# Kernel tuning notes

Hardware: AMD Instinct MI355X
Metric: run time of the kernel (lower is better)

Reference implementation:

```python
import jax, jax.numpy as jnp
import numpy as np

N = 50000      # nodes
E = 400000     # edges (avg degree 8)
N_IN = 256     # n_in_chan
N_HID = 256    # n_hid_chan


def gcn_conv(x, src, dst, W, b, n):
    """PyG GCNConv: D^{-1/2}(A+I)D^{-1/2} X W^T + b (add_self_loops=True, unit weights)."""
    h = x @ W.T                                           # [n, out]
    # degree over A + I: each node has a self loop (the initial ones) plus in-edges
    deg = jnp.ones((n,), h.dtype).at[dst].add(1.0)        # [n]
    dinv = jax.lax.rsqrt(deg)                             # deg >= 1 always
    norm = dinv[src] * dinv[dst]                          # [E]
    agg = jnp.zeros_like(h).at[dst].add(h[src] * norm[:, None])
    agg = agg + h * (dinv * dinv)[:, None]                # self-loop term, norm = dinv_i^2
    return agg + b


def setup_inputs() -> dict:
    key = jax.random.key(0)
    k1, k2, k3, k4 = jax.random.split(key, 4)
    x = jax.random.normal(k1, (N, N_IN + N_HID), dtype=jnp.float32)
    edge_index = jax.random.randint(k2, (2, E), 0, N, dtype=jnp.int64)
    s1 = 1.0 / np.sqrt(N_IN + N_HID)
    s2 = 1.0 / np.sqrt(N_HID)
    W1 = jax.random.normal(k3, (N_HID, N_IN + N_HID), dtype=jnp.float32) * s1
    W2 = jax.random.normal(k4, (N_HID, N_HID), dtype=jnp.float32) * s2
    b1 = jnp.zeros((N_HID,), jnp.float32)
    b2 = jnp.zeros((N_HID,), jnp.float32)
    return {"x": x, "edge_index": edge_index, "W1": W1, "b1": b1, "W2": W2, "b2": b2}


def reference(x, edge_index, W1, b1, W2, b2):
    src, dst = edge_index[0], edge_index[1]
    h = jax.nn.relu(gcn_conv(x, src, dst, W1, b1, N))
    return gcn_conv(h, src, dst, W2, b2, N)
```

## Files before the change

kernel.cpp:

```cpp
#include <hip/hip_runtime.h>
#include <hip/hip_bf16.h>

#define NN 50000
#define CH 256
#define SLOTS 96
#define G1K 512
#define G2K 256

typedef unsigned short u16;
typedef unsigned int   u32;

using short8 = __attribute__((ext_vector_type(8))) short;
using u16x8  = __attribute__((ext_vector_type(8))) unsigned short;
using f32x4  = __attribute__((ext_vector_type(4))) float;

static __device__ __forceinline__ float4 ld4(const float* p){ return *(const float4*)p; }

static __device__ __forceinline__ u16 f2b(float f){
  u32 u = __float_as_uint(f);
  u = (u + 0x7fffu + ((u >> 16) & 1u)) >> 16;
  return (u16)u;
}
static __device__ __forceinline__ float b2f(u16 b){
  return __uint_as_float(((u32)b) << 16);
}
static __device__ __forceinline__ int pkbf(float lo, float hi){
  __hip_bfloat162 h = __float22bfloat162_rn(make_float2(lo, hi));
  int r; __builtin_memcpy(&r, &h, 4); return r;
}

static __device__ __forceinline__ void gload_lds16(const u16* g, u16* l){
  __builtin_amdgcn_global_load_lds((const __attribute__((address_space(1))) void*)g,
                                   (__attribute__((address_space(3))) void*)l, 16, 0, 0);
}

#define WBAR(vm) do{ \
    asm volatile("s_waitcnt vmcnt(" #vm ") lgkmcnt(0)" ::: "memory"); \
    __builtin_amdgcn_s_barrier(); \
  }while(0)


__global__ void ell_build_kernel(const int* __restrict__ src, const int* __restrict__ dst,
                                 int* __restrict__ deg, int* __restrict__ ell, int E,
                                 const float* __restrict__ W1, u16* __restrict__ W1bf, int w1n4,
                                 const float* __restrict__ W2, u16* __restrict__ W2bf, int w2n4){
  int T = gridDim.x * 256;
  int g = blockIdx.x*256 + threadIdx.x;
  if (g < E){
    int d = dst[g];
    int pos = atomicAdd(&deg[d], 1);
    if (pos < SLOTS) ell[(size_t)d*SLOTS + pos] = src[g];
  }
  for (int i = g; i < w1n4; i += T){
    float4 v = ld4(W1 + (size_t)i*4);
    ushort4 o; o.x=f2b(v.x); o.y=f2b(v.y); o.z=f2b(v.z); o.w=f2b(v.w);
    *(ushort4*)(W1bf + (size_t)i*4) = o;
  }
  for (int i = g; i < w2n4; i += T){
    float4 v = ld4(W2 + (size_t)i*4);
    ushort4 o; o.x=f2b(v.x); o.y=f2b(v.y); o.z=f2b(v.z); o.w=f2b(v.w);
    *(ushort4*)(W2bf + (size_t)i*4) = o;
  }
}


#define G1_GLB(kt, bb) do{ \
    gload_lds16(gb0 + (kt)*32, &Bs[bb][wave*512]); \
    gload_lds16(gb1 + (kt)*32, &Bs[bb][2048 + wave*512]); \
  }while(0)

#define G1_LA(S, k0) do{ \
    A##S##a = ld4(ga0 + (k0)); A##S##b = ld4(ga0 + (k0) + 4); \
    A##S##c = ld4(ga1 + (k0)); A##S##d = ld4(ga1 + (k0) + 4); \
  }while(0)

#define G1_SA(S) do{ \
    int4 _w0 = { pkbf(A##S##a.x,A##S##a.y), pkbf(A##S##a.z,A##S##a.w), \
                 pkbf(A##S##b.x,A##S##b.y), pkbf(A##S##b.z,A##S##b.w) }; \
    int4 _w1 = { pkbf(A##S##c.x,A##S##c.y), pkbf(A##S##c.z,A##S##c.w), \
                 pkbf(A##S##d.x,A##S##d.y), pkbf(A##S##d.z,A##S##d.w) }; \
    *(int4*)&As[S][aoff0] = _w0; \
    *(int4*)&As[S][aoff1] = _w1; \
  }while(0)

#define G1_COMP(ra, rb) do{ \
    short8 af[4], bq[4]; \
    _Pragma("unroll") \
    for (int i=0;i<4;i++) af[i] = *(const short8*)&As[ra][(wm*64 + i*16 + lm)*32 + lk]; \
    _Pragma("unroll") \
    for (int j=0;j<4;j++) bq[j] = *(const short8*)&Bs[rb][(wn*64 + j*16 + lm)*32 + lk]; \
    _Pragma("unroll") \
    for (int i=0;i<4;i++) \
      _Pragma("unroll") \
      for (int j=0;j<4;j++) \
        acc[i][j] = __builtin_amdgcn_mfma_f32_16x16x32_bf16(af[i], bq[j], acc[i][j], 0, 0, 0); \
  }while(0)

#define G1_BODY(t, ra, rb, ss, wb, vm) do{ \
    if ((t)+2 < 16) G1_GLB((t)+2, wb); \
    G1_COMP(ra, rb); \
    if ((t)+1 < 16) G1_SA(ss); \
    if ((t)+3 < 16) G1_LA(ss, ((t)+3)*32); \
    WBAR(vm); \
  }while(0)

__global__ __launch_bounds__(256) void gemm1_kernel(const float* __restrict__ A,
                                                    const u16* __restrict__ Bbf,
                                                    u16* __restrict__ C, int M){
  __shared__ u16 As[2][128*32];
  __shared__ u16 Bs[4][128*32];
  int tid = threadIdx.x;
  int wave = tid >> 6, lane = tid & 63;
  int bm = blockIdx.x, bn = blockIdx.y;

  int sr = tid >> 2;
  int sc = (tid & 3) * 8;
  int ar0 = bm*128 + sr;       if (ar0 > M-1) ar0 = M-1;
  int ar1 = bm*128 + 64 + sr;  if (ar1 > M-1) ar1 = M-1;
  const float* ga0 = A + (size_t)ar0*G1K + sc;
  const float* ga1 = A + (size_t)ar1*G1K + sc;
  const u16*   gb0 = Bbf + (size_t)(bn*128 + sr)*G1K + sc;
  const u16*   gb1 = gb0 + (size_t)64*G1K;
  int aoff0 = sr*32 + sc;
  int aoff1 = (64+sr)*32 + sc;

  int wm = wave & 1, wn = wave >> 1;
  int lm = lane & 15;
  int lk = (lane >> 4) * 8;

  f32x4 acc[4][4] = {};

  float4 A0a,A0b,A0c,A0d;
  float4 A1a,A1b,A1c,A1d;

  G1_LA(0, 0);
  G1_GLB(0, 0);
  G1_LA(1, 32);
  G1_GLB(1, 1);
  asm volatile("s_waitcnt vmcnt(0)" ::: "memory");
  G1_SA(0);
  G1_LA(0, 64);
  asm volatile("s_waitcnt lgkmcnt(0)" ::: "memory");
  __builtin_amdgcn_s_barrier();

  G1_BODY( 0, 0,0, 1, 2, 6);
  G1_BODY( 1, 1,1, 0, 3, 6);
  G1_BODY( 2, 0,2, 1, 0, 6);
  G1_BODY( 3, 1,3, 0, 1, 6);
  G1_BODY( 4, 0,0, 1, 2, 6);
  G1_BODY( 5, 1,1, 0, 3, 6);
  G1_BODY( 6, 0,2, 1, 0, 6);
  G1_BODY( 7, 1,3, 0, 1, 6);
  G1_BODY( 8, 0,0, 1, 2, 6);
  G1_BODY( 9, 1,1, 0, 3, 6);
  G1_BODY(10, 0,2, 1, 0, 6);
  G1_BODY(11, 1,3, 0, 1, 6);
  G1_BODY(12, 0,0, 1, 2, 6);
  G1_BODY(13, 1,1, 0, 3, 2);
  G1_BODY(14, 0,2, 1, 0, 0);
  G1_COMP(1, 3);

  int rb = (lane >> 4) * 4;
  #pragma unroll
  for (int i=0;i<4;i++){
    #pragma unroll
    for (int r=0;r<4;r++){
      int row = bm*128 + wm*64 + i*16 + rb + r;
      if (row < M){
        #pragma unroll
        for (int j=0;j<4;j++){
          int col = bn*128 + wn*64 + j*16 + lm;
          C[(size_t)row*CH + col] = f2b(acc[i][j][r]);
        }
      }
    }
  }
}


#define G2_GLB(kt, bb) do{ \
    gload_lds16(ga0 + (kt)*32, &As2[bb][wave*512]); \
    gload_lds16(ga1 + (kt)*32, &As2[bb][2048 + wave*512]); \
    gload_lds16(gb0 + (kt)*32, &Bs2[bb][wave*512]); \
    gload_lds16(gb1 + (kt)*32, &Bs2[bb][2048 + wave*512]); \
  }while(0)

#define G2_COMP(rb) do{ \
    short8 af[4], bq[4]; \
    _Pragma("unroll") \
    for (int i=0;i<4;i++) af[i] = *(const short8*)&As2[rb][(wm*64 + i*16 + lm)*32 + lk]; \
    _Pragma("unroll") \
    for (int j=0;j<4;j++) bq[j] = *(const short8*)&Bs2[rb][(wn*64 + j*16 + lm)*32 + lk]; \
    _Pragma("unroll") \
    for (int i=0;i<4;i++) \
      _Pragma("unroll") \
      for (int j=0;j<4;j++) \
        acc[i][j] = __builtin_amdgcn_mfma_f32_16x16x32_bf16(af[i], bq[j], acc[i][j], 0, 0, 0); \
  }while(0)

__global__ __launch_bounds__(256) void gemm2_kernel(const u16* __restrict__ A,
                                                    const u16* __restrict__ B,
                                                    u16* __restrict__ C, int M){
  __shared__ u16 As2[4][128*32];
  __shared__ u16 Bs2[4][128*32];
  int tid = threadIdx.x;
  int wave = tid >> 6, lane = tid & 63;
  int bm = blockIdx.x, bn = blockIdx.y;

  int sr = tid >> 2;
  int sc = (tid & 3) * 8;
  int ar0 = bm*128 + sr;       if (ar0 > M-1) ar0 = M-1;
  int ar1 = bm*128 + 64 + sr;  if (ar1 > M-1) ar1 = M-1;
  const u16* ga0 = A + (size_t)ar0*G2K + sc;
  const u16* ga1 = A + (size_t)ar1*G2K + sc;
  const u16* gb0 = B + (size_t)(bn*128 + sr)*G2K + sc;
  const u16* gb1 = gb0 + (size_t)64*G2K;

  int wm = wave & 1, wn = wave >> 1;
  int lm = lane & 15;
  int lk = (lane >> 4) * 8;

  f32x4 acc[4][4] = {};

  G2_GLB(0, 0);
  G2_GLB(1, 1);
  asm volatile("s_waitcnt vmcnt(0)" ::: "memory");
  __builtin_amdgcn_s_barrier();

  G2_GLB(2, 2); G2_COMP(0); WBAR(4);
  G2_GLB(3, 3); G2_COMP(1); WBAR(4);
  G2_GLB(4, 0); G2_COMP(2); WBAR(4);
  G2_GLB(5, 1); G2_COMP(3); WBAR(4);
  G2_GLB(6, 2); G2_COMP(0); WBAR(4);
  G2_GLB(7, 3); G2_COMP(1); WBAR(4);
                G2_COMP(2); WBAR(0);
                G2_COMP(3);

  int rb = (lane >> 4) * 4;
  #pragma unroll
  for (int i=0;i<4;i++){
    #pragma unroll
    for (int r=0;r<4;r++){
      int row = bm*128 + wm*64 + i*16 + rb + r;
      if (row < M){
        #pragma unroll
        for (int j=0;j<4;j++){
          int col = bn*128 + wn*64 + j*16 + lm;
          C[(size_t)row*CH + col] = f2b(acc[i][j][r]);
        }
      }
    }
  }
}


template<bool RELU, bool OUTBF>
__global__ __launch_bounds__(256) void aggregate_kernel(const u16* __restrict__ h,
                                                        const float* __restrict__ bias,
                                                        const int* __restrict__ deg,
                                                        const int* __restrict__ ell,
                                                        void* __restrict__ outv, int n){
  int wave = threadIdx.x >> 6;
  int lane = threadIdx.x & 63;
  int i = blockIdx.x*4 + wave;
  if (i >= n) return;
  int half = lane >> 5;
  int c = (lane & 31) * 8;

  int degi = deg[i];
  float di = rsqrtf(1.0f + (float)degi);
  int m = degi < SLOTS ? degi : SLOTS;
  const int* row = ell + (size_t)i*SLOTS;

  float acc[8];
  #pragma unroll
  for (int k=0;k<8;k++) acc[k] = 0.f;

  int e = half;
  for (; e + 6 < m; e += 8){
    int s0 = row[e],   s1 = row[e+2], s2 = row[e+4], s3 = row[e+6];
    float n0 = rsqrtf(1.0f + (float)deg[s0]) * di;
    float n1 = rsqrtf(1.0f + (float)deg[s1]) * di;
    float n2 = rsqrtf(1.0f + (float)deg[s2]) * di;
    float n3 = rsqrtf(1.0f + (float)deg[s3]) * di;
    u16x8 h0 = *(const u16x8*)(h + (size_t)s0*CH + c);
    u16x8 h1 = *(const u16x8*)(h + (size_t)s1*CH + c);
    u16x8 h2 = *(const u16x8*)(h + (size_t)s2*CH + c);
    u16x8 h3 = *(const u16x8*)(h + (size_t)s3*CH + c);
    #pragma unroll
    for (int k=0;k<8;k++) acc[k] += b2f(h0[k])*n0;
    #pragma unroll
    for (int k=0;k<8;k++) acc[k] += b2f(h1[k])*n1;
    #pragma unroll
    for (int k=0;k<8;k++) acc[k] += b2f(h2[k])*n2;
    #pragma unroll
    for (int k=0;k<8;k++) acc[k] += b2f(h3[k])*n3;
  }
  for (; e < m; e += 2){
    int s0 = row[e];
    float n0 = rsqrtf(1.0f + (float)deg[s0]) * di;
    u16x8 h0 = *(const u16x8*)(h + (size_t)s0*CH + c);
    #pragma unroll
    for (int k=0;k<8;k++) acc[k] += b2f(h0[k])*n0;
  }

  if (half == 0){
    float w = di*di;
    float4 b0 = ld4(bias + c), b1 = ld4(bias + c + 4);
    u16x8 hv = *(const u16x8*)(h + (size_t)i*CH + c);
    acc[0] += b2f(hv[0])*w + b0.x; acc[1] += b2f(hv[1])*w + b0.y;
    acc[2] += b2f(hv[2])*w + b0.z; acc[3] += b2f(hv[3])*w + b0.w;
    acc[4] += b2f(hv[4])*w + b1.x; acc[5] += b2f(hv[5])*w + b1.y;
    acc[6] += b2f(hv[6])*w + b1.z; acc[7] += b2f(hv[7])*w + b1.w;
  }

  #pragma unroll
  for (int k=0;k<8;k++) acc[k] += __shfl_xor(acc[k], 32, 64);

  if (half == 0){
    if (RELU){
      #pragma unroll
      for (int k=0;k<8;k++) acc[k] = fmaxf(acc[k], 0.f);
    }
    if (OUTBF){
      u16x8 o;
      #pragma unroll
      for (int k=0;k<8;k++) o[k] = f2b(acc[k]);
      *(u16x8*)((u16*)outv + (size_t)i*CH + c) = o;
    } else {
      float* op = (float*)outv + (size_t)i*CH + c;
      *(float4*)op       = make_float4(acc[0],acc[1],acc[2],acc[3]);
      *(float4*)(op + 4) = make_float4(acc[4],acc[5],acc[6],acc[7]);
    }
  }
}


extern "C" void kernel_launch(void* const* d_in, const int* in_sizes, int n_in,
                              void* d_out, int out_size, void* d_ws, size_t ws_size,
                              hipStream_t stream){
  const float* x  = (const float*)d_in[0];
  const int*   ei = (const int*)d_in[1];
  const float* W1 = (const float*)d_in[2];
  const float* b1 = (const float*)d_in[3];
  const float* W2 = (const float*)d_in[4];
  const float* b2 = (const float*)d_in[5];
  float* out = (float*)d_out;

  const int n = NN;
  const int E = in_sizes[1] / 2;
  const int* src = ei;
  const int* dst = ei + E;

  char* ws = (char*)d_ws;
  size_t off = 0;
  auto alloc = [&](size_t bytes)->char* {
    char* p = ws + off;
    off += (bytes + 255) & ~(size_t)255;
    return p;
  };
  u16*   h1bf   = (u16*)  alloc((size_t)n*CH*sizeof(u16));
  u16*   g2out  = (u16*)  alloc((size_t)n*CH*sizeof(u16));
  u16*   W1bf   = (u16*)  alloc((size_t)CH*G1K*sizeof(u16));
  u16*   W2bf   = (u16*)  alloc((size_t)CH*CH*sizeof(u16));
  int*   deg    = (int*)  alloc((size_t)n*sizeof(int));
  int*   ell    = (int*)  alloc((size_t)n*SLOTS*sizeof(int));
  (void)ws_size;

  u16* g1out = (u16*)d_out;

  hipMemsetAsync(deg, 0, (size_t)n*sizeof(int), stream);
  ell_build_kernel<<<(E+255)/256, 256, 0, stream>>>(src, dst, deg, ell, E,
                                                    W1, W1bf, CH*G1K/4,
                                                    W2, W2bf, CH*CH/4);

  dim3 gg((n+127)/128, CH/128);
  gemm1_kernel<<<gg, 256, 0, stream>>>(x, W1bf, g1out, n);
  aggregate_kernel<true, true><<<(n+3)/4, 256, 0, stream>>>(g1out, b1, deg, ell, h1bf, n);

  gemm2_kernel<<<gg, 256, 0, stream>>>(h1bf, W2bf, g2out, n);
  aggregate_kernel<false, false><<<(n+3)/4, 256, 0, stream>>>(g2out, b2, deg, ell, out, n);
}
```

Before: 313.3 us.

## Use 512-thread blocks in both GEMMs, halving per-wave output tiles

```diff
diff --git a/kernel.cpp b/kernel.cpp
--- a/kernel.cpp
+++ b/kernel.cpp
@@ -64,49 +64,34 @@
 }
 
 
-#define G1_GLB(kt, bb) do{ \
-    gload_lds16(gb0 + (kt)*32, &Bs[bb][wave*512]); \
-    gload_lds16(gb1 + (kt)*32, &Bs[bb][2048 + wave*512]); \
-  }while(0)
+#define G1_GLB(kt, bb) gload_lds16(gb + (kt)*32, &Bs[bb][wave*512])
 
 #define G1_LA(S, k0) do{ \
-    A##S##a = ld4(ga0 + (k0)); A##S##b = ld4(ga0 + (k0) + 4); \
-    A##S##c = ld4(ga1 + (k0)); A##S##d = ld4(ga1 + (k0) + 4); \
+    A##S##a = ld4(ga + (k0)); A##S##b = ld4(ga + (k0) + 4); \
   }while(0)
 
 #define G1_SA(S) do{ \
-    int4 _w0 = { pkbf(A##S##a.x,A##S##a.y), pkbf(A##S##a.z,A##S##a.w), \
-                 pkbf(A##S##b.x,A##S##b.y), pkbf(A##S##b.z,A##S##b.w) }; \
-    int4 _w1 = { pkbf(A##S##c.x,A##S##c.y), pkbf(A##S##c.z,A##S##c.w), \
-                 pkbf(A##S##d.x,A##S##d.y), pkbf(A##S##d.z,A##S##d.w) }; \
-    *(int4*)&As[S][aoff0] = _w0; \
-    *(int4*)&As[S][aoff1] = _w1; \
+    int4 _w = { pkbf(A##S##a.x,A##S##a.y), pkbf(A##S##a.z,A##S##a.w), \
+                pkbf(A##S##b.x,A##S##b.y), pkbf(A##S##b.z,A##S##b.w) }; \
+    *(int4*)&As[S][aoff] = _w; \
   }while(0)
 
 #define G1_COMP(ra, rb) do{ \
-    short8 af[4], bq[4]; \
+    short8 af[4], bq[2]; \
     _Pragma("unroll") \
     for (int i=0;i<4;i++) af[i] = *(const short8*)&As[ra][(wm*64 + i*16 + lm)*32 + lk]; \
     _Pragma("unroll") \
-    for (int j=0;j<4;j++) bq[j] = *(const short8*)&Bs[rb][(wn*64 + j*16 + lm)*32 + lk]; \
+    for (int j=0;j<2;j++) bq[j] = *(const short8*)&Bs[rb][(wn*32 + j*16 + lm)*32 + lk]; \
     _Pragma("unroll") \
     for (int i=0;i<4;i++) \
       _Pragma("unroll") \
-      for (int j=0;j<4;j++) \
+      for (int j=0;j<2;j++) \
         acc[i][j] = __builtin_amdgcn_mfma_f32_16x16x32_bf16(af[i], bq[j], acc[i][j], 0, 0, 0); \
   }while(0)
 
-#define G1_BODY(t, ra, rb, ss, wb, vm) do{ \
-    if ((t)+2 < 16) G1_GLB((t)+2, wb); \
-    G1_COMP(ra, rb); \
-    if ((t)+1 < 16) G1_SA(ss); \
-    if ((t)+3 < 16) G1_LA(ss, ((t)+3)*32); \
-    WBAR(vm); \
-  }while(0)
-
-__global__ __launch_bounds__(256) void gemm1_kernel(const float* __restrict__ A,
-                                                    const u16* __restrict__ Bbf,
-                                                    u16* __restrict__ C, int M){
+__global__ __launch_bounds__(512, 4) void gemm1_kernel(const float* __restrict__ A,
+                                                       const u16* __restrict__ Bbf,
+                                                       u16* __restrict__ C, int M){
   __shared__ u16 As[2][128*32];
   __shared__ u16 Bs[4][128*32];
   int tid = threadIdx.x;
@@ -115,50 +100,45 @@
 
   int sr = tid >> 2;
   int sc = (tid & 3) * 8;
-  int ar0 = bm*128 + sr;       if (ar0 > M-1) ar0 = M-1;
-  int ar1 = bm*128 + 64 + sr;  if (ar1 > M-1) ar1 = M-1;
-  const float* ga0 = A + (size_t)ar0*G1K + sc;
-  const float* ga1 = A + (size_t)ar1*G1K + sc;
-  const u16*   gb0 = Bbf + (size_t)(bn*128 + sr)*G1K + sc;
-  const u16*   gb1 = gb0 + (size_t)64*G1K;
-  int aoff0 = sr*32 + sc;
-  int aoff1 = (64+sr)*32 + sc;
+  int ar = bm*128 + sr; if (ar > M-1) ar = M-1;
+  const float* ga = A + (size_t)ar*G1K + sc;
+  const u16*   gb = Bbf + (size_t)(bn*128 + sr)*G1K + sc;
+  int aoff = sr*32 + sc;
 
   int wm = wave & 1, wn = wave >> 1;
   int lm = lane & 15;
   int lk = (lane >> 4) * 8;
 
-  f32x4 acc[4][4] = {};
-
-  float4 A0a,A0b,A0c,A0d;
-  float4 A1a,A1b,A1c,A1d;
+  f32x4 acc[4][2] = {};
+
+  float4 A0a,A0b;
+  float4 A1a,A1b;
 
   G1_LA(0, 0);
   G1_GLB(0, 0);
   G1_LA(1, 32);
   G1_GLB(1, 1);
-  asm volatile("s_waitcnt vmcnt(0)" ::: "memory");
   G1_SA(0);
   G1_LA(0, 64);
-  asm volatile("s_waitcnt lgkmcnt(0)" ::: "memory");
+  asm volatile("s_waitcnt vmcnt(0) lgkmcnt(0)" ::: "memory");
   __builtin_amdgcn_s_barrier();
 
-  G1_BODY( 0, 0,0, 1, 2, 6);
-  G1_BODY( 1, 1,1, 0, 3, 6);
-  G1_BODY( 2, 0,2, 1, 0, 6);
-  G1_BODY( 3, 1,3, 0, 1, 6);
-  G1_BODY( 4, 0,0, 1, 2, 6);
-  G1_BODY( 5, 1,1, 0, 3, 6);
-  G1_BODY( 6, 0,2, 1, 0, 6);
-  G1_BODY( 7, 1,3, 0, 1, 6);
-  G1_BODY( 8, 0,0, 1, 2, 6);
-  G1_BODY( 9, 1,1, 0, 3, 6);
-  G1_BODY(10, 0,2, 1, 0, 6);
-  G1_BODY(11, 1,3, 0, 1, 6);
-  G1_BODY(12, 0,0, 1, 2, 6);
-  G1_BODY(13, 1,1, 0, 3, 2);
-  G1_BODY(14, 0,2, 1, 0, 0);
-  G1_COMP(1, 3);
+  G1_GLB( 2,2); G1_COMP(0,0); G1_SA(1); G1_LA(1, 96); WBAR(3);
+  G1_GLB( 3,3); G1_COMP(1,1); G1_SA(0); G1_LA(0,128); WBAR(3);
+  G1_GLB( 4,0); G1_COMP(0,2); G1_SA(1); G1_LA(1,160); WBAR(3);
+  G1_GLB( 5,1); G1_COMP(1,3); G1_SA(0); G1_LA(0,192); WBAR(3);
+  G1_GLB( 6,2); G1_COMP(0,0); G1_SA(1); G1_LA(1,224); WBAR(3);
+  G1_GLB( 7,3); G1_COMP(1,1); G1_SA(0); G1_LA(0,256); WBAR(3);
+  G1_GLB( 8,0); G1_COMP(0,2); G1_SA(1); G1_LA(1,288); WBAR(3);
+  G1_GLB( 9,1); G1_COMP(1,3); G1_SA(0); G1_LA(0,320); WBAR(3);
+  G1_GLB(10,2); G1_COMP(0,0); G1_SA(1); G1_LA(1,352); WBAR(3);
+  G1_GLB(11,3); G1_COMP(1,1); G1_SA(0); G1_LA(0,384); WBAR(3);
+  G1_GLB(12,0); G1_COMP(0,2); G1_SA(1); G1_LA(1,416); WBAR(3);
+  G1_GLB(13,1); G1_COMP(1,3); G1_SA(0); G1_LA(0,448); WBAR(3);
+  G1_GLB(14,2); G1_COMP(0,0); G1_SA(1); G1_LA(1,480); WBAR(3);
+  G1_GLB(15,3); G1_COMP(1,1); G1_SA(0);               WBAR(1);
+                G1_COMP(0,2); G1_SA(1);               WBAR(0);
+                G1_COMP(1,3);
 
   int rb = (lane >> 4) * 4;
   #pragma unroll
@@ -168,8 +148,8 @@
       int row = bm*128 + wm*64 + i*16 + rb + r;
       if (row < M){
         #pragma unroll
-        for (int j=0;j<4;j++){
-          int col = bn*128 + wn*64 + j*16 + lm;
+        for (int j=0;j<2;j++){
+          int col = bn*128 + wn*32 + j*16 + lm;
           C[(size_t)row*CH + col] = f2b(acc[i][j][r]);
         }
       }
@@ -179,28 +159,26 @@
 
 
 #define G2_GLB(kt, bb) do{ \
-    gload_lds16(ga0 + (kt)*32, &As2[bb][wave*512]); \
-    gload_lds16(ga1 + (kt)*32, &As2[bb][2048 + wave*512]); \
-    gload_lds16(gb0 + (kt)*32, &Bs2[bb][wave*512]); \
-    gload_lds16(gb1 + (kt)*32, &Bs2[bb][2048 + wave*512]); \
+    gload_lds16(ga + (kt)*32, &As2[bb][wave*512]); \
+    gload_lds16(gb + (kt)*32, &Bs2[bb][wave*512]); \
   }while(0)
 
 #define G2_COMP(rb) do{ \
-    short8 af[4], bq[4]; \
+    short8 af[4], bq[2]; \
     _Pragma("unroll") \
     for (int i=0;i<4;i++) af[i] = *(const short8*)&As2[rb][(wm*64 + i*16 + lm)*32 + lk]; \
     _Pragma("unroll") \
-    for (int j=0;j<4;j++) bq[j] = *(const short8*)&Bs2[rb][(wn*64 + j*16 + lm)*32 + lk]; \
+    for (int j=0;j<2;j++) bq[j] = *(const short8*)&Bs2[rb][(wn*32 + j*16 + lm)*32 + lk]; \
     _Pragma("unroll") \
     for (int i=0;i<4;i++) \
       _Pragma("unroll") \
-      for (int j=0;j<4;j++) \
+      for (int j=0;j<2;j++) \
         acc[i][j] = __builtin_amdgcn_mfma_f32_16x16x32_bf16(af[i], bq[j], acc[i][j], 0, 0, 0); \
   }while(0)
 
-__global__ __launch_bounds__(256) void gemm2_kernel(const u16* __restrict__ A,
-                                                    const u16* __restrict__ B,
-                                                    u16* __restrict__ C, int M){
+__global__ __launch_bounds__(512, 4) void gemm2_kernel(const u16* __restrict__ A,
+                                                       const u16* __restrict__ B,
+                                                       u16* __restrict__ C, int M){
   __shared__ u16 As2[4][128*32];
   __shared__ u16 Bs2[4][128*32];
   int tid = threadIdx.x;
@@ -209,30 +187,27 @@
 
   int sr = tid >> 2;
   int sc = (tid & 3) * 8;
-  int ar0 = bm*128 + sr;       if (ar0 > M-1) ar0 = M-1;
-  int ar1 = bm*128 + 64 + sr;  if (ar1 > M-1) ar1 = M-1;
-  const u16* ga0 = A + (size_t)ar0*G2K + sc;
-  const u16* ga1 = A + (size_t)ar1*G2K + sc;
-  const u16* gb0 = B + (size_t)(bn*128 + sr)*G2K + sc;
-  const u16* gb1 = gb0 + (size_t)64*G2K;
+  int ar = bm*128 + sr; if (ar > M-1) ar = M-1;
+  const u16* ga = A + (size_t)ar*G2K + sc;
+  const u16* gb = B + (size_t)(bn*128 + sr)*G2K + sc;
 
   int wm = wave & 1, wn = wave >> 1;
   int lm = lane & 15;
   int lk = (lane >> 4) * 8;
 
-  f32x4 acc[4][4] = {};
+  f32x4 acc[4][2] = {};
 
   G2_GLB(0, 0);
   G2_GLB(1, 1);
   asm volatile("s_waitcnt vmcnt(0)" ::: "memory");
   __builtin_amdgcn_s_barrier();
 
-  G2_GLB(2, 2); G2_COMP(0); WBAR(4);
-  G2_GLB(3, 3); G2_COMP(1); WBAR(4);
-  G2_GLB(4, 0); G2_COMP(2); WBAR(4);
-  G2_GLB(5, 1); G2_COMP(3); WBAR(4);
-  G2_GLB(6, 2); G2_COMP(0); WBAR(4);
-  G2_GLB(7, 3); G2_COMP(1); WBAR(4);
+  G2_GLB(2, 2); G2_COMP(0); WBAR(2);
+  G2_GLB(3, 3); G2_COMP(1); WBAR(2);
+  G2_GLB(4, 0); G2_COMP(2); WBAR(2);
+  G2_GLB(5, 1); G2_COMP(3); WBAR(2);
+  G2_GLB(6, 2); G2_COMP(0); WBAR(2);
+  G2_GLB(7, 3); G2_COMP(1); WBAR(2);
                 G2_COMP(2); WBAR(0);
                 G2_COMP(3);
 
@@ -244,8 +219,8 @@
       int row = bm*128 + wm*64 + i*16 + rb + r;
       if (row < M){
         #pragma unroll
-        for (int j=0;j<4;j++){
-          int col = bn*128 + wn*64 + j*16 + lm;
+        for (int j=0;j<2;j++){
+          int col = bn*128 + wn*32 + j*16 + lm;
           C[(size_t)row*CH + col] = f2b(acc[i][j][r]);
         }
       }
@@ -375,9 +350,9 @@
                                                     W2, W2bf, CH*CH/4);
 
   dim3 gg((n+127)/128, CH/128);
-  gemm1_kernel<<<gg, 256, 0, stream>>>(x, W1bf, g1out, n);
+  gemm1_kernel<<<gg, 512, 0, stream>>>(x, W1bf, g1out, n);
   aggregate_kernel<true, true><<<(n+3)/4, 256, 0, stream>>>(g1out, b1, deg, ell, h1bf, n);
 
-  gemm2_kernel<<<gg, 256, 0, stream>>>(h1bf, W2bf, g2out, n);
+  gemm2_kernel<<<gg, 512, 0, stream>>>(h1bf, W2bf, g2out, n);
   aggregate_kernel<false, false><<<(n+3)/4, 256, 0, stream>>>(g2out, b2, deg, ell, out, n);
 }
```

Result: no change. 313.4 us (+0.0%).
